# Kernel optimization log

Hardware: AMD Instinct MI355X
Metric: run time of the kernel (lower is better)

The kernel has to match this reference:

```python
import jax, jax.numpy as jnp
import numpy as np

B, S, D, H, E, K = 4, 2048, 768, 3072, 8, 2
LB_SCALE = 0.01
NOISY_STD = 1.0


def setup_inputs() -> dict:
    key = jax.random.key(0)
    ks = jax.random.split(key, 8)
    x = jax.random.normal(ks[0], (B, S, D), jnp.float32)
    # gate_linear: nn.Linear(D, E, bias=False); torch weight is [E, D]
    gate_w = jax.random.normal(ks[1], (E, D), jnp.float32) * 0.02
    noise_weight = jnp.zeros((E,), jnp.float32)  # initialized to zeros in torch
    noise = jax.random.normal(ks[2], (B, S, E), jnp.float32)  # torch.randn_like(logits)
    # expert weights stored in (in, out) layout: y = x @ w + b
    w1 = jax.random.normal(ks[3], (E, D, H), jnp.float32) * 0.02
    b1 = jnp.zeros((E, H), jnp.float32)
    w2 = jax.random.normal(ks[4], (E, D, H), jnp.float32) * 0.02
    b2 = jnp.zeros((E, H), jnp.float32)
    wp = jax.random.normal(ks[5], (E, H, D), jnp.float32) * 0.02
    bp = jnp.zeros((E, D), jnp.float32)
    return {"x": x, "gate_w": gate_w, "noise_weight": noise_weight, "noise": noise,
            "w1": w1, "b1": b1, "w2": w2, "b2": b2, "wp": wp, "bp": bp}


def reference(x, gate_w, noise_weight, noise, w1, b1, w2, b2, wp, bp):
    num_experts = gate_w.shape[0]
    # --- TopKGateParallel ---
    logits = jnp.einsum('bsd,ed->bse', x, gate_w)            # [B,S,E]
    gate_weights = jax.nn.softmax(logits, axis=-1)
    gate_weights_mean = gate_weights.reshape(-1, num_experts).mean(0)
    uniform = 1.0 / num_experts
    load_balance_loss = jnp.mean((gate_weights_mean - uniform) ** 2) * LB_SCALE
    logits_noisy = logits + noise * NOISY_STD * noise_weight  # noise_weight zeros => no-op at init
    top_k_vals, top_k_ids = jax.lax.top_k(logits_noisy, K)    # [B,S,K]
    # scatter top-k back into a -inf tensor, then softmax -> sparse gates
    topk_mask = jax.nn.one_hot(top_k_ids, num_experts, dtype=logits.dtype).sum(-2) > 0  # [B,S,E]
    sparse_logits = jnp.where(topk_mask, logits_noisy, -jnp.inf)
    gates = jax.nn.softmax(sparse_logits, axis=-1)            # zeros outside top-k
    # --- per-expert SwiGLU, weighted combine (gates are exactly 0 off top-k) ---
    y = jnp.zeros_like(x)
    for e in range(num_experts):  # small fixed expert count
        h = (x @ w1[e] + b1[e]) * jax.nn.silu(x @ w2[e] + b2[e])  # [B,S,H]
        y = y + gates[..., e:e + 1] * (h @ wp[e] + bp[e])
    return y, load_balance_loss
```

## Files before the change

### kernel.cpp

```cpp
#include <hip/hip_runtime.h>
#include <hip/hip_bf16.h>

#define NTOK 8192
#define DDIM 768
#define HDIM 3072
#define NEXP 8
#define MROWS (NTOK*2)

typedef float f32x4 __attribute__((ext_vector_type(4)));
typedef short bf16x8 __attribute__((ext_vector_type(8)));
typedef unsigned short u16x4 __attribute__((ext_vector_type(4)));

__device__ __forceinline__ unsigned short f2bf(float f) {
  union { float f; unsigned u; } v; v.f = f;
  unsigned r = v.u + 0x7fffu + ((v.u >> 16) & 1u);
  return (unsigned short)(r >> 16);
}

typedef __attribute__((address_space(3))) unsigned int* lds_ptr_t;
typedef const __attribute__((address_space(1))) unsigned int* gbl_ptr_t;
__device__ __forceinline__ void async16(const void* g, void* l) {
  __builtin_amdgcn_global_load_lds((gbl_ptr_t)g, (lds_ptr_t)l, 16, 0, 0);
}

__global__ __launch_bounds__(128) void gating_kernel(
    const float* __restrict__ x, const float* __restrict__ gw,
    const float* __restrict__ nw, const float* __restrict__ noise,
    int* counts, float* sums, int* tok_list, float* gate_list,
    int* tok_top, float* gate_top, int* pos_top)
{
  __shared__ float s_gw[NEXP*DDIM];
  __shared__ float s_sums[NEXP];
  __shared__ float s_nw[NEXP];
  int tid = threadIdx.x;
  for (int i = tid; i < NEXP*DDIM/4; i += 128)
    ((f32x4*)s_gw)[i] = ((const f32x4*)gw)[i];
  if (tid < NEXP) { s_sums[tid] = 0.f; s_nw[tid] = nw[tid]; }
  __syncthreads();
  int t = blockIdx.x*128 + tid;
  float acc[NEXP];
  #pragma unroll
  for (int e = 0; e < NEXP; ++e) acc[e] = 0.f;
  const f32x4* xr = (const f32x4*)(x + (size_t)t*DDIM);
  for (int d4 = 0; d4 < DDIM/4; ++d4) {
    f32x4 xv = xr[d4];
    #pragma unroll
    for (int e = 0; e < NEXP; ++e) {
      f32x4 g = *(const f32x4*)&s_gw[e*DDIM + d4*4];
      acc[e] += xv.x*g.x + xv.y*g.y + xv.z*g.z + xv.w*g.w;
    }
  }
  float m = acc[0];
  #pragma unroll
  for (int e = 1; e < NEXP; ++e) m = fmaxf(m, acc[e]);
  float p[NEXP], s = 0.f;
  #pragma unroll
  for (int e = 0; e < NEXP; ++e) { p[e] = __expf(acc[e]-m); s += p[e]; }
  float inv = 1.f/s;
  #pragma unroll
  for (int e = 0; e < NEXP; ++e) atomicAdd(&s_sums[e], p[e]*inv);
  float ln[NEXP];
  #pragma unroll
  for (int e = 0; e < NEXP; ++e) ln[e] = acc[e] + noise[(size_t)t*NEXP+e]*s_nw[e];
  int i0 = 0; float v0 = ln[0];
  #pragma unroll
  for (int e = 1; e < NEXP; ++e) if (ln[e] > v0) { v0 = ln[e]; i0 = e; }
  int i1 = -1; float v1 = 0.f;
  #pragma unroll
  for (int e = 0; e < NEXP; ++e)
    if (e != i0 && (i1 < 0 || ln[e] > v1)) { v1 = ln[e]; i1 = e; }
  float e1 = __expf(v1 - v0);
  float g0 = 1.f/(1.f + e1);
  float g1 = e1*g0;
  int p0 = atomicAdd(&counts[i0], 1);
  tok_list[i0*NTOK + p0] = t; gate_list[i0*NTOK + p0] = g0;
  int p1 = atomicAdd(&counts[i1], 1);
  tok_list[i1*NTOK + p1] = t; gate_list[i1*NTOK + p1] = g1;
  tok_top[2*t] = i0; tok_top[2*t+1] = i1;
  gate_top[2*t] = g0; gate_top[2*t+1] = g1;
  pos_top[2*t] = p0; pos_top[2*t+1] = p1;
  __syncthreads();
  if (tid < NEXP) atomicAdd(&sums[tid], s_sums[tid]);
}

__global__ void finalize_kernel(const int* counts, const float* sums,
                                int* offsets, float* loss_out)
{
  if (threadIdx.x == 0) {
    int o = 0;
    #pragma unroll
    for (int e = 0; e < NEXP; ++e) { offsets[e] = o; o += counts[e]; }
    offsets[NEXP] = o;
    float l = 0.f;
    #pragma unroll
    for (int e = 0; e < NEXP; ++e) {
      float dv = sums[e]*(1.f/(float)NTOK) - 1.f/(float)NEXP;
      l += dv*dv;
    }
    loss_out[0] = l*(0.01f/(float)NEXP);
  }
}

__global__ __launch_bounds__(256) void cvt_x_kernel(const float* __restrict__ x,
                                                    unsigned short* __restrict__ xb)
{
  int i = blockIdx.x*256 + threadIdx.x;
  f32x4 v = ((const f32x4*)x)[i];
  u16x4 o; o.x = f2bf(v.x); o.y = f2bf(v.y); o.z = f2bf(v.z); o.w = f2bf(v.w);
  ((u16x4*)xb)[i] = o;
}

__global__ __launch_bounds__(256) void transpose_cvt2_kernel(
    const float* __restrict__ src1, unsigned short* __restrict__ dst1,
    const float* __restrict__ src2, unsigned short* __restrict__ dst2,
    int R, int C)
{
  __shared__ unsigned short s[64*65];
  int z = blockIdx.z;
  int e = z & (NEXP-1);
  const float* src = (z < NEXP) ? src1 : src2;
  unsigned short* dst = (z < NEXP) ? dst1 : dst2;
  int r0 = blockIdx.y*64, c0 = blockIdx.x*64;
  const float* sp = src + ((size_t)e*R + r0)*C + c0;
  unsigned short* dp = dst + ((size_t)e*C + c0)*R + r0;
  int t = threadIdx.x;
  #pragma unroll
  for (int i = 0; i < 16; ++i) {
    int idx = t + 256*i;
    int r = idx >> 6, c = idx & 63;
    s[c*65 + r] = f2bf(sp[(size_t)r*C + c]);
  }
  __syncthreads();
  #pragma unroll
  for (int i = 0; i < 16; ++i) {
    int idx = t + 256*i;
    int c = idx >> 6, r = idx & 63;
    dp[(size_t)c*R + r] = s[c*65 + r];
  }
}

__global__ __launch_bounds__(256) void transpose_cvt_kernel(
    const float* __restrict__ src, unsigned short* __restrict__ dst, int R, int C)
{
  __shared__ unsigned short s[64*65];
  int e = blockIdx.z;
  int r0 = blockIdx.y*64, c0 = blockIdx.x*64;
  const float* sp = src + ((size_t)e*R + r0)*C + c0;
  unsigned short* dp = dst + ((size_t)e*C + c0)*R + r0;
  int t = threadIdx.x;
  #pragma unroll
  for (int i = 0; i < 16; ++i) {
    int idx = t + 256*i;
    int r = idx >> 6, c = idx & 63;
    s[c*65 + r] = f2bf(sp[(size_t)r*C + c]);
  }
  __syncthreads();
  #pragma unroll
  for (int i = 0; i < 16; ++i) {
    int idx = t + 256*i;
    int c = idx >> 6, r = idx & 63;
    dp[(size_t)c*R + r] = s[c*65 + r];
  }
}

__global__ __launch_bounds__(256) void compact_kernel(
    const int* __restrict__ counts, const int* __restrict__ offsets,
    const int* __restrict__ tok_list, const float* __restrict__ gate_list,
    int* __restrict__ row_token, float* __restrict__ row_gate)
{
  int e = blockIdx.y;
  int pos = blockIdx.x*256 + threadIdx.x;
  if (pos < counts[e]) {
    int r = offsets[e] + pos;
    row_token[r] = tok_list[e*NTOK + pos];
    row_gate[r]  = gate_list[e*NTOK + pos];
  }
}

__global__ __launch_bounds__(256) void init_y_kernel(
    const int* __restrict__ tok_top, const float* __restrict__ gate_top,
    const float* __restrict__ bp, float* __restrict__ y)
{
  int i = blockIdx.x*256 + threadIdx.x;
  int t = i / (DDIM/4);
  int d4 = i % (DDIM/4);
  int e0 = tok_top[2*t], e1 = tok_top[2*t+1];
  float g0 = gate_top[2*t], g1 = gate_top[2*t+1];
  f32x4 b0 = ((const f32x4*)(bp + (size_t)e0*DDIM))[d4];
  f32x4 b1v = ((const f32x4*)(bp + (size_t)e1*DDIM))[d4];
  ((f32x4*)y)[i] = g0*b0 + g1*b1v;
}

__global__ __launch_bounds__(256) void ffn1_mfma(
    const unsigned short* __restrict__ xb,
    const unsigned short* __restrict__ w1T, const unsigned short* __restrict__ w2T,
    const float* __restrict__ b1, const float* __restrict__ b2,
    const int* __restrict__ offsets, const int* __restrict__ row_token,
    unsigned short* __restrict__ h_buf, int h_base, int HC)
{
  int e = blockIdx.z;
  int r_lo = offsets[e];
  int rows_e = offsets[e+1] - r_lo;
  int bx = blockIdx.x;
  if (bx*128 >= rows_e) return;
  int r0 = r_lo + bx*128;
  int rows_valid = rows_e - bx*128; if (rows_valid > 128) rows_valid = 128;
  int h0 = h_base + blockIdx.y*64;

  __shared__ __align__(16) char sA[16384];
  __shared__ __align__(16) char sB[16384];
  __shared__ int s_tok[128];

  int tid = threadIdx.x;
  if (tid < 128) {
    int r = r0 + tid; if (r > MROWS-1) r = MROWS-1;
    s_tok[tid] = row_token[r];
  }
  __syncthreads();

  int lane = tid & 63, w = tid >> 6;
  int l16 = lane & 15, quad = lane >> 4;
  int lr = lane >> 2, ls = lane & 3;

  const unsigned short* gA[4]; char* lA[4];
  const unsigned short* gB[4]; char* lB[4];
  #pragma unroll
  for (int i = 0; i < 4; ++i) {
    int slot = i*4 + w;
    int chunk = slot & 7, kh = slot >> 3;
    gA[i] = xb + (size_t)s_tok[chunk*16 + lr]*DDIM + kh*32 + ls*8;
    lA[i] = sA + slot*1024;
    int mat = (slot >> 2) & 1;
    int col = h0 + w*16 + lr;
    const unsigned short* base = mat ? w2T : w1T;
    gB[i] = base + ((size_t)e*HDIM + col)*DDIM + kh*32 + ls*8;
    lB[i] = sB + slot*1024;
  }

  f32x4 acc1[8], acc2[8];
  #pragma unroll
  for (int i = 0; i < 8; ++i) { acc1[i] = (f32x4){0,0,0,0}; acc2[i] = (f32x4){0,0,0,0}; }

  int fro = l16*64 + quad*16;

  for (int k0 = 0; k0 < DDIM; k0 += 64) {
    #pragma unroll
    for (int i = 0; i < 4; ++i) async16(gA[i] + k0, lA[i]);
    #pragma unroll
    for (int i = 0; i < 4; ++i) async16(gB[i] + k0, lB[i]);
    __syncthreads();
    #pragma unroll
    for (int kh = 0; kh < 2; ++kh) {
      bf16x8 bf1 = *(const bf16x8*)(sB + (kh*8 + w)*1024 + fro);
      bf16x8 bf2 = *(const bf16x8*)(sB + (kh*8 + 4 + w)*1024 + fro);
      #pragma unroll
      for (int mt = 0; mt < 8; ++mt) {
        bf16x8 af = *(const bf16x8*)(sA + (kh*8 + mt)*1024 + fro);
        acc1[mt] = __builtin_amdgcn_mfma_f32_16x16x32_bf16(af, bf1, acc1[mt], 0, 0, 0);
        acc2[mt] = __builtin_amdgcn_mfma_f32_16x16x32_bf16(af, bf2, acc2[mt], 0, 0, 0);
      }
    }
    __syncthreads();
  }
  int hcol = h0 + w*16 + l16;
  float bb1 = b1[(size_t)e*HDIM + hcol];
  float bb2 = b2[(size_t)e*HDIM + hcol];
  int hl = hcol - h_base;
  #pragma unroll
  for (int mt = 0; mt < 8; ++mt) {
    #pragma unroll
    for (int r = 0; r < 4; ++r) {
      int row = mt*16 + quad*4 + r;
      if (row < rows_valid) {
        float c1 = acc1[mt][r] + bb1;
        float c2 = acc2[mt][r] + bb2;
        float hv = c1 * (c2 / (1.f + __expf(-c2)));
        h_buf[(size_t)(r0 + row)*HC + hl] = f2bf(hv);
      }
    }
  }
}

__global__ __launch_bounds__(256) void ffn2_mfma(
    const unsigned short* __restrict__ h_buf, const unsigned short* __restrict__ wpT,
    const int* __restrict__ offsets, const int* __restrict__ row_token,
    const float* __restrict__ row_gate, float* __restrict__ outp,
    int h_base, int HC, int mode)
{
  int e = blockIdx.z;
  int r_lo = offsets[e];
  int rows_e = offsets[e+1] - r_lo;
  int bx = blockIdx.x;
  if (bx*128 >= rows_e) return;
  int r0 = r_lo + bx*128;
  int rows_valid = rows_e - bx*128; if (rows_valid > 128) rows_valid = 128;
  int c0 = blockIdx.y*128;

  __shared__ __align__(16) char sA[16384];
  __shared__ __align__(16) char sB[16384];
  __shared__ int s_tok[128];
  __shared__ float s_gate[128];

  int tid = threadIdx.x;
  if (tid < 128) {
    int r = r0 + tid; if (r > MROWS-1) r = MROWS-1;
    s_tok[tid]  = row_token[r];
    s_gate[tid] = row_gate[r];
  }
  __syncthreads();

  int lane = tid & 63, w = tid >> 6;
  int l16 = lane & 15, quad = lane >> 4;
  int lr = lane >> 2, ls = lane & 3;
  int wr = w & 1, wcg = w >> 1;

  const unsigned short* gA[4]; char* lA[4];
  const unsigned short* gB[4]; char* lB[4];
  #pragma unroll
  for (int i = 0; i < 4; ++i) {
    int slot = i*4 + w;
    int chunk = slot & 7, kh = slot >> 3;
    int rr = r0 + chunk*16 + lr; if (rr > MROWS-1) rr = MROWS-1;
    gA[i] = h_buf + (size_t)rr*HC + kh*32 + ls*8;
    lA[i] = sA + slot*1024;
    int col = c0 + chunk*16 + lr;
    gB[i] = wpT + ((size_t)e*DDIM + col)*HDIM + h_base + kh*32 + ls*8;
    lB[i] = sB + slot*1024;
  }

  f32x4 acc[4][4];
  #pragma unroll
  for (int i = 0; i < 4; ++i)
    #pragma unroll
    for (int j = 0; j < 4; ++j) acc[i][j] = (f32x4){0,0,0,0};

  int fro = l16*64 + quad*16;

  for (int k0 = 0; k0 < HC; k0 += 64) {
    #pragma unroll
    for (int i = 0; i < 4; ++i) async16(gA[i] + k0, lA[i]);
    #pragma unroll
    for (int i = 0; i < 4; ++i) async16(gB[i] + k0, lB[i]);
    __syncthreads();
    #pragma unroll
    for (int kh = 0; kh < 2; ++kh) {
      bf16x8 bfr[4];
      #pragma unroll
      for (int nt = 0; nt < 4; ++nt)
        bfr[nt] = *(const bf16x8*)(sB + (kh*8 + wcg*4 + nt)*1024 + fro);
      #pragma unroll
      for (int mt = 0; mt < 4; ++mt) {
        bf16x8 af = *(const bf16x8*)(sA + (kh*8 + wr*4 + mt)*1024 + fro);
        #pragma unroll
        for (int nt = 0; nt < 4; ++nt)
          acc[mt][nt] = __builtin_amdgcn_mfma_f32_16x16x32_bf16(af, bfr[nt], acc[mt][nt], 0, 0, 0);
      }
    }
    __syncthreads();
  }

  if (mode == 0) {
    #pragma unroll
    for (int nt = 0; nt < 4; ++nt) {
      int col = c0 + wcg*64 + nt*16 + l16;
      #pragma unroll
      for (int mt = 0; mt < 4; ++mt) {
        #pragma unroll
        for (int r = 0; r < 4; ++r) {
          int row = wr*64 + mt*16 + quad*4 + r;
          if (row < rows_valid)
            outp[(size_t)(r0 + row)*DDIM + col] = acc[mt][nt][r];
        }
      }
    }
  } else {
    #pragma unroll
    for (int nt = 0; nt < 4; ++nt) {
      int col = c0 + wcg*64 + nt*16 + l16;
      #pragma unroll
      for (int mt = 0; mt < 4; ++mt) {
        #pragma unroll
        for (int r = 0; r < 4; ++r) {
          int row = wr*64 + mt*16 + quad*4 + r;
          if (row < rows_valid)
            atomicAdd(&outp[(size_t)s_tok[row]*DDIM + col], s_gate[row]*acc[mt][nt][r]);
        }
      }
    }
  }
}

__global__ __launch_bounds__(256) void combine_kernel(
    const float* __restrict__ part, const int* __restrict__ tok_top,
    const float* __restrict__ gate_top, const int* __restrict__ pos_top,
    const int* __restrict__ offsets, const float* __restrict__ bp,
    float* __restrict__ y)
{
  int i = blockIdx.x*256 + threadIdx.x;
  int t = i / (DDIM/4);
  int d4 = i % (DDIM/4);
  int e0 = tok_top[2*t], e1 = tok_top[2*t+1];
  float g0 = gate_top[2*t], g1 = gate_top[2*t+1];
  int r0 = offsets[e0] + pos_top[2*t];
  int r1 = offsets[e1] + pos_top[2*t+1];
  f32x4 v0 = ((const f32x4*)part)[(size_t)r0*(DDIM/4) + d4];
  f32x4 v1 = ((const f32x4*)part)[(size_t)r1*(DDIM/4) + d4];
  f32x4 b0 = ((const f32x4*)(bp + (size_t)e0*DDIM))[d4];
  f32x4 b1v = ((const f32x4*)(bp + (size_t)e1*DDIM))[d4];
  ((f32x4*)y)[i] = g0*(v0 + b0) + g1*(v1 + b1v);
}

__global__ __launch_bounds__(256) void ffn2_kernel(
    const unsigned short* __restrict__ h_buf, const float* __restrict__ wp,
    const int* __restrict__ offsets, const int* __restrict__ row_token,
    const float* __restrict__ row_gate, float* __restrict__ y, int h_base, int HC)
{
  int e = blockIdx.z;
  int r_lo = offsets[e];
  int rows_e = offsets[e+1] - r_lo;
  int bx = blockIdx.x;
  if (bx*128 >= rows_e) return;
  int r0 = r_lo + bx*128;
  int rows_valid = rows_e - bx*128; if (rows_valid > 128) rows_valid = 128;
  int c0 = blockIdx.y*128;

  __shared__ unsigned short sA[128*40];
  __shared__ int s_tok[128];
  __shared__ float s_gate[128];

  int tid = threadIdx.x;
  if (tid < 128) {
    int r = r0 + tid; if (r > MROWS-1) r = MROWS-1;
    s_tok[tid]  = row_token[r];
    s_gate[tid] = row_gate[r];
  }
  int lane = tid & 63;
  int wc = tid >> 6;
  int quad = lane >> 4, l16 = lane & 15;

  const float* wp0 = wp + (size_t)e*HDIM*DDIM + c0 + wc*32 + l16;

  f32x4 acc[8][2];
  #pragma unroll
  for (int i = 0; i < 8; ++i) { acc[i][0] = (f32x4){0,0,0,0}; acc[i][1] = (f32x4){0,0,0,0}; }
  __syncthreads();

  for (int k0 = 0; k0 < HC; k0 += 32) {
    #pragma unroll
    for (int i = 0; i < 2; ++i) {
      int c = i*256 + tid;
      int row = c >> 2, k8 = c & 3;
      int rr = r0 + row; if (rr > MROWS-1) rr = MROWS-1;
      bf16x8 v = *(const bf16x8*)(h_buf + (size_t)rr*HC + k0 + k8*8);
      *(bf16x8*)&sA[row*40 + k8*8] = v;
    }
    float bv[2][8];
    #pragma unroll
    for (int nt = 0; nt < 2; ++nt)
      #pragma unroll
      for (int j = 0; j < 8; ++j)
        bv[nt][j] = wp0[(size_t)(h_base + k0 + quad*8 + j)*DDIM + nt*16];
    bf16x8 bfr[2];
    #pragma unroll
    for (int nt = 0; nt < 2; ++nt)
      #pragma unroll
      for (int j = 0; j < 8; ++j) bfr[nt][j] = (short)f2bf(bv[nt][j]);
    __syncthreads();
    #pragma unroll
    for (int mt = 0; mt < 8; ++mt) {
      bf16x8 af = *(const bf16x8*)&sA[(mt*16 + l16)*40 + quad*8];
      acc[mt][0] = __builtin_amdgcn_mfma_f32_16x16x32_bf16(af, bfr[0], acc[mt][0], 0, 0, 0);
      acc[mt][1] = __builtin_amdgcn_mfma_f32_16x16x32_bf16(af, bfr[1], acc[mt][1], 0, 0, 0);
    }
    __syncthreads();
  }
  #pragma unroll
  for (int nt = 0; nt < 2; ++nt) {
    int col = c0 + wc*32 + nt*16 + l16;
    #pragma unroll
    for (int mt = 0; mt < 8; ++mt) {
      #pragma unroll
      for (int r = 0; r < 4; ++r) {
        int row = mt*16 + quad*4 + r;
        if (row < rows_valid)
          atomicAdd(&y[(size_t)s_tok[row]*DDIM + col], s_gate[row]*acc[mt][nt][r]);
      }
    }
  }
}

extern "C" void kernel_launch(void* const* d_in, const int* in_sizes, int n_in,
                              void* d_out, int out_size, void* d_ws, size_t ws_size,
                              hipStream_t stream)
{
  (void)in_sizes; (void)n_in; (void)out_size;
  const float* x     = (const float*)d_in[0];
  const float* gw    = (const float*)d_in[1];
  const float* nw    = (const float*)d_in[2];
  const float* noise = (const float*)d_in[3];
  const float* w1    = (const float*)d_in[4];
  const float* b1    = (const float*)d_in[5];
  const float* w2    = (const float*)d_in[6];
  const float* b2    = (const float*)d_in[7];
  const float* wp    = (const float*)d_in[8];
  const float* bp    = (const float*)d_in[9];
  float* y = (float*)d_out;

  char* ws = (char*)d_ws;
  int*   counts   = (int*)(ws + 0);
  float* sums     = (float*)(ws + 64);
  int*   offsets  = (int*)(ws + 128);
  size_t off = 256;
  int*   tok_list  = (int*)(ws + off);   off += (size_t)NEXP*NTOK*4;
  float* gate_list = (float*)(ws + off); off += (size_t)NEXP*NTOK*4;
  int*   tok_top   = (int*)(ws + off);   off += (size_t)NTOK*2*4;
  float* gate_top  = (float*)(ws + off); off += (size_t)NTOK*2*4;
  int*   pos_top   = (int*)(ws + off);   off += (size_t)NTOK*2*4;
  int*   row_token = (int*)(ws + off);   off += (size_t)MROWS*4;
  float* row_gate  = (float*)(ws + off); off += (size_t)MROWS*4;
  unsigned short* xb = (unsigned short*)(ws + off); off += (size_t)NTOK*DDIM*2;

  const size_t WT    = (size_t)NEXP*DDIM*HDIM*2;
  const size_t HFULL = (size_t)MROWS*HDIM*2;
  const size_t PSZ   = (size_t)MROWS*DDIM*4;

  unsigned short* w1T = (unsigned short*)(ws + off);
  unsigned short* w2T = (unsigned short*)(ws + off + WT);
  unsigned short* wpT = (unsigned short*)(ws + off + 2*WT);

  bool tierA = (off + 3*WT + HFULL + PSZ <= ws_size);
  bool haveP = (off + 3*WT + (size_t)MROWS*128*2 <= ws_size);
  size_t oH = off + (haveP ? 3*WT : 2*WT);

  int HC;
  unsigned short* h_buf;
  float* part = nullptr;
  if (tierA) {
    HC = HDIM;
    h_buf = (unsigned short*)(ws + off + 3*WT);
    part  = (float*)(ws + off + 3*WT + HFULL);
  } else {
    static const int hc_opts[6] = {3072, 1536, 768, 384, 192, 128};
    HC = 128;
    for (int i = 0; i < 6; ++i)
      if (oH + (size_t)MROWS*hc_opts[i]*2 <= ws_size) { HC = hc_opts[i]; break; }
    h_buf = (unsigned short*)(ws + oH);
  }

  hipMemsetAsync(d_ws, 0, 256, stream);
  cvt_x_kernel<<<NTOK*DDIM/1024, 256, 0, stream>>>(x, xb);
  transpose_cvt2_kernel<<<dim3(HDIM/64, DDIM/64, NEXP*2), 256, 0, stream>>>(
      w1, w1T, w2, w2T, DDIM, HDIM);
  if (haveP)
    transpose_cvt_kernel<<<dim3(DDIM/64, HDIM/64, NEXP), 256, 0, stream>>>(wp, wpT, HDIM, DDIM);

  gating_kernel<<<NTOK/128, 128, 0, stream>>>(x, gw, nw, noise, counts, sums,
                                              tok_list, gate_list, tok_top, gate_top, pos_top);
  finalize_kernel<<<1, 64, 0, stream>>>(counts, sums, offsets, y + (size_t)NTOK*DDIM);
  compact_kernel<<<dim3(NTOK/256, NEXP), 256, 0, stream>>>(counts, offsets, tok_list,
                                                           gate_list, row_token, row_gate);

  if (tierA) {
    ffn1_mfma<<<dim3(128, HDIM/64, NEXP), 256, 0, stream>>>(xb, w1T, w2T, b1, b2, offsets,
                                                            row_token, h_buf, 0, HC);
    ffn2_mfma<<<dim3(128, DDIM/128, NEXP), 256, 0, stream>>>(h_buf, wpT, offsets, row_token,
                                                             row_gate, part, 0, HC, 0);
    combine_kernel<<<NTOK*DDIM/1024, 256, 0, stream>>>(part, tok_top, gate_top, pos_top,
                                                       offsets, bp, y);
  } else {
    init_y_kernel<<<NTOK*DDIM/1024, 256, 0, stream>>>(tok_top, gate_top, bp, y);
    int nch = HDIM / HC;
    for (int c = 0; c < nch; ++c) {
      ffn1_mfma<<<dim3(128, HC/64, NEXP), 256, 0, stream>>>(xb, w1T, w2T, b1, b2, offsets,
                                                            row_token, h_buf, c*HC, HC);
      if (haveP)
        ffn2_mfma<<<dim3(128, DDIM/128, NEXP), 256, 0, stream>>>(h_buf, wpT, offsets, row_token,
                                                                 row_gate, y, c*HC, HC, 1);
      else
        ffn2_kernel<<<dim3(128, DDIM/128, NEXP), 256, 0, stream>>>(h_buf, wp, offsets, row_token,
                                                                   row_gate, y, c*HC, HC);
    }
  }
}
```

Measured before the change: 1.006 ms.

## Use persistent row-block loops, XOR-swizzled LDS, and K=32 steps in expert GEMMs

The grouped FFN GEMM kernels now launch a compact 1D grid: the expert index is interleaved into the block id, and each block loops over row blocks with a stride of 32. This replaces the old 128-row-block grid, in which most blocks returned immediately. The K step drops from 64 to 32, halving LDS tiles to 8KB so more blocks can fit per CU. An XOR swizzle on the global load segment and the fragment read offset is meant to avoid LDS bank conflicts. The trade-off is twice as many barrier pairs per K, and a block serialises its row blocks whenever an expert receives more than 32 of them.

```diff
diff --git a/kernel.cpp b/kernel.cpp
--- a/kernel.cpp
+++ b/kernel.cpp
@@ -6,6 +6,7 @@
 #define HDIM 3072
 #define NEXP 8
 #define MROWS (NTOK*2)
+#define RBMAX 32
 
 typedef float f32x4 __attribute__((ext_vector_type(4)));
 typedef short bf16x8 __attribute__((ext_vector_type(8)));
@@ -198,84 +199,82 @@
     const int* __restrict__ offsets, const int* __restrict__ row_token,
     unsigned short* __restrict__ h_buf, int h_base, int HC)
 {
-  int e = blockIdx.z;
+  int id = blockIdx.x;
+  int e = id & 7;
+  int s = id >> 3;
+  int rb0 = s & (RBMAX-1);
+  int cg = s >> 5;
   int r_lo = offsets[e];
   int rows_e = offsets[e+1] - r_lo;
-  int bx = blockIdx.x;
-  if (bx*128 >= rows_e) return;
-  int r0 = r_lo + bx*128;
-  int rows_valid = rows_e - bx*128; if (rows_valid > 128) rows_valid = 128;
-  int h0 = h_base + blockIdx.y*64;
-
-  __shared__ __align__(16) char sA[16384];
-  __shared__ __align__(16) char sB[16384];
+  int h0 = h_base + cg*64;
+
+  __shared__ __align__(16) char sA[8192];
+  __shared__ __align__(16) char sB[8192];
   __shared__ int s_tok[128];
 
   int tid = threadIdx.x;
-  if (tid < 128) {
-    int r = r0 + tid; if (r > MROWS-1) r = MROWS-1;
-    s_tok[tid] = row_token[r];
-  }
-  __syncthreads();
-
   int lane = tid & 63, w = tid >> 6;
   int l16 = lane & 15, quad = lane >> 4;
   int lr = lane >> 2, ls = lane & 3;
-
-  const unsigned short* gA[4]; char* lA[4];
-  const unsigned short* gB[4]; char* lB[4];
-  #pragma unroll
-  for (int i = 0; i < 4; ++i) {
-    int slot = i*4 + w;
-    int chunk = slot & 7, kh = slot >> 3;
-    gA[i] = xb + (size_t)s_tok[chunk*16 + lr]*DDIM + kh*32 + ls*8;
-    lA[i] = sA + slot*1024;
-    int mat = (slot >> 2) & 1;
-    int col = h0 + w*16 + lr;
-    const unsigned short* base = mat ? w2T : w1T;
-    gB[i] = base + ((size_t)e*HDIM + col)*DDIM + kh*32 + ls*8;
-    lB[i] = sB + slot*1024;
-  }
-
-  f32x4 acc1[8], acc2[8];
-  #pragma unroll
-  for (int i = 0; i < 8; ++i) { acc1[i] = (f32x4){0,0,0,0}; acc2[i] = (f32x4){0,0,0,0}; }
-
-  int fro = l16*64 + quad*16;
-
-  for (int k0 = 0; k0 < DDIM; k0 += 64) {
-    #pragma unroll
-    for (int i = 0; i < 4; ++i) async16(gA[i] + k0, lA[i]);
-    #pragma unroll
-    for (int i = 0; i < 4; ++i) async16(gB[i] + k0, lB[i]);
-    __syncthreads();
-    #pragma unroll
-    for (int kh = 0; kh < 2; ++kh) {
-      bf16x8 bf1 = *(const bf16x8*)(sB + (kh*8 + w)*1024 + fro);
-      bf16x8 bf2 = *(const bf16x8*)(sB + (kh*8 + 4 + w)*1024 + fro);
-      #pragma unroll
-      for (int mt = 0; mt < 8; ++mt) {
-        bf16x8 af = *(const bf16x8*)(sA + (kh*8 + mt)*1024 + fro);
-        acc1[mt] = __builtin_amdgcn_mfma_f32_16x16x32_bf16(af, bf1, acc1[mt], 0, 0, 0);
-        acc2[mt] = __builtin_amdgcn_mfma_f32_16x16x32_bf16(af, bf2, acc2[mt], 0, 0, 0);
-      }
-    }
-    __syncthreads();
-  }
+  int kseg = ls ^ (lr & 3);
+  int fro = l16*64 + ((quad ^ (l16 & 3)) << 4);
+
+  int colB = h0 + w*16 + lr;
+  const unsigned short* gB1 = w1T + ((size_t)e*HDIM + colB)*DDIM + kseg*8;
+  const unsigned short* gB2 = w2T + ((size_t)e*HDIM + colB)*DDIM + kseg*8;
+  char* lA0 = sA + w*1024;
+  char* lA1 = sA + (w+4)*1024;
+  char* lB1 = sB + w*1024;
+  char* lB2 = sB + (w+4)*1024;
+
   int hcol = h0 + w*16 + l16;
   float bb1 = b1[(size_t)e*HDIM + hcol];
   float bb2 = b2[(size_t)e*HDIM + hcol];
   int hl = hcol - h_base;
-  #pragma unroll
-  for (int mt = 0; mt < 8; ++mt) {
-    #pragma unroll
-    for (int r = 0; r < 4; ++r) {
-      int row = mt*16 + quad*4 + r;
-      if (row < rows_valid) {
-        float c1 = acc1[mt][r] + bb1;
-        float c2 = acc2[mt][r] + bb2;
-        float hv = c1 * (c2 / (1.f + __expf(-c2)));
-        h_buf[(size_t)(r0 + row)*HC + hl] = f2bf(hv);
+
+  for (int rb = rb0; rb*128 < rows_e; rb += RBMAX) {
+    int r0 = r_lo + rb*128;
+    int rows_valid = rows_e - rb*128; if (rows_valid > 128) rows_valid = 128;
+    __syncthreads();
+    if (tid < 128) {
+      int r = r0 + tid; if (r > MROWS-1) r = MROWS-1;
+      s_tok[tid] = row_token[r];
+    }
+    __syncthreads();
+    const unsigned short* gA0 = xb + (size_t)s_tok[w*16 + lr]*DDIM + kseg*8;
+    const unsigned short* gA1 = xb + (size_t)s_tok[(w+4)*16 + lr]*DDIM + kseg*8;
+
+    f32x4 acc1[8], acc2[8];
+    #pragma unroll
+    for (int i = 0; i < 8; ++i) { acc1[i] = (f32x4){0,0,0,0}; acc2[i] = (f32x4){0,0,0,0}; }
+
+    for (int k0 = 0; k0 < DDIM; k0 += 32) {
+      async16(gA0 + k0, lA0);
+      async16(gA1 + k0, lA1);
+      async16(gB1 + k0, lB1);
+      async16(gB2 + k0, lB2);
+      __syncthreads();
+      bf16x8 bf1 = *(const bf16x8*)(sB + w*1024 + fro);
+      bf16x8 bf2 = *(const bf16x8*)(sB + (w+4)*1024 + fro);
+      #pragma unroll
+      for (int mt = 0; mt < 8; ++mt) {
+        bf16x8 af = *(const bf16x8*)(sA + mt*1024 + fro);
+        acc1[mt] = __builtin_amdgcn_mfma_f32_16x16x32_bf16(af, bf1, acc1[mt], 0, 0, 0);
+        acc2[mt] = __builtin_amdgcn_mfma_f32_16x16x32_bf16(af, bf2, acc2[mt], 0, 0, 0);
+      }
+      __syncthreads();
+    }
+    #pragma unroll
+    for (int mt = 0; mt < 8; ++mt) {
+      #pragma unroll
+      for (int r = 0; r < 4; ++r) {
+        int row = mt*16 + quad*4 + r;
+        if (row < rows_valid) {
+          float c1 = acc1[mt][r] + bb1;
+          float c2 = acc2[mt][r] + bb2;
+          float hv = c1 * (c2 / (1.f + __expf(-c2)));
+          h_buf[(size_t)(r0 + row)*HC + hl] = f2bf(hv);
+        }
       }
     }
   }
@@ -287,103 +286,102 @@
     const float* __restrict__ row_gate, float* __restrict__ outp,
     int h_base, int HC, int mode)
 {
-  int e = blockIdx.z;
+  int id = blockIdx.x;
+  int e = id & 7;
+  int s = id >> 3;
+  int rb0 = s & (RBMAX-1);
+  int cb = s >> 5;
   int r_lo = offsets[e];
   int rows_e = offsets[e+1] - r_lo;
-  int bx = blockIdx.x;
-  if (bx*128 >= rows_e) return;
-  int r0 = r_lo + bx*128;
-  int rows_valid = rows_e - bx*128; if (rows_valid > 128) rows_valid = 128;
-  int c0 = blockIdx.y*128;
-
-  __shared__ __align__(16) char sA[16384];
-  __shared__ __align__(16) char sB[16384];
+  int c0 = cb*128;
+
+  __shared__ __align__(16) char sA[8192];
+  __shared__ __align__(16) char sB[8192];
   __shared__ int s_tok[128];
   __shared__ float s_gate[128];
 
   int tid = threadIdx.x;
-  if (tid < 128) {
-    int r = r0 + tid; if (r > MROWS-1) r = MROWS-1;
-    s_tok[tid]  = row_token[r];
-    s_gate[tid] = row_gate[r];
-  }
-  __syncthreads();
-
   int lane = tid & 63, w = tid >> 6;
   int l16 = lane & 15, quad = lane >> 4;
   int lr = lane >> 2, ls = lane & 3;
+  int kseg = ls ^ (lr & 3);
+  int fro = l16*64 + ((quad ^ (l16 & 3)) << 4);
   int wr = w & 1, wcg = w >> 1;
 
-  const unsigned short* gA[4]; char* lA[4];
-  const unsigned short* gB[4]; char* lB[4];
-  #pragma unroll
-  for (int i = 0; i < 4; ++i) {
-    int slot = i*4 + w;
-    int chunk = slot & 7, kh = slot >> 3;
-    int rr = r0 + chunk*16 + lr; if (rr > MROWS-1) rr = MROWS-1;
-    gA[i] = h_buf + (size_t)rr*HC + kh*32 + ls*8;
-    lA[i] = sA + slot*1024;
-    int col = c0 + chunk*16 + lr;
-    gB[i] = wpT + ((size_t)e*DDIM + col)*HDIM + h_base + kh*32 + ls*8;
-    lB[i] = sB + slot*1024;
-  }
-
-  f32x4 acc[4][4];
-  #pragma unroll
-  for (int i = 0; i < 4; ++i)
-    #pragma unroll
-    for (int j = 0; j < 4; ++j) acc[i][j] = (f32x4){0,0,0,0};
-
-  int fro = l16*64 + quad*16;
-
-  for (int k0 = 0; k0 < HC; k0 += 64) {
-    #pragma unroll
-    for (int i = 0; i < 4; ++i) async16(gA[i] + k0, lA[i]);
-    #pragma unroll
-    for (int i = 0; i < 4; ++i) async16(gB[i] + k0, lB[i]);
+  const unsigned short* gB0 = wpT + ((size_t)e*DDIM + c0 + w*16 + lr)*HDIM + h_base + kseg*8;
+  const unsigned short* gB1 = wpT + ((size_t)e*DDIM + c0 + (w+4)*16 + lr)*HDIM + h_base + kseg*8;
+  char* lA0 = sA + w*1024;
+  char* lA1 = sA + (w+4)*1024;
+  char* lB0 = sB + w*1024;
+  char* lB1 = sB + (w+4)*1024;
+
+  for (int rb = rb0; rb*128 < rows_e; rb += RBMAX) {
+    int r0 = r_lo + rb*128;
+    int rows_valid = rows_e - rb*128; if (rows_valid > 128) rows_valid = 128;
     __syncthreads();
-    #pragma unroll
-    for (int kh = 0; kh < 2; ++kh) {
+    if (tid < 128) {
+      int r = r0 + tid; if (r > MROWS-1) r = MROWS-1;
+      s_tok[tid]  = row_token[r];
+      s_gate[tid] = row_gate[r];
+    }
+    __syncthreads();
+    int rA0 = r0 + w*16 + lr;     if (rA0 > MROWS-1) rA0 = MROWS-1;
+    int rA1 = r0 + (w+4)*16 + lr; if (rA1 > MROWS-1) rA1 = MROWS-1;
+    const unsigned short* gA0 = h_buf + (size_t)rA0*HC + kseg*8;
+    const unsigned short* gA1 = h_buf + (size_t)rA1*HC + kseg*8;
+
+    f32x4 acc[4][4];
+    #pragma unroll
+    for (int i = 0; i < 4; ++i)
+      #pragma unroll
+      for (int j = 0; j < 4; ++j) acc[i][j] = (f32x4){0,0,0,0};
+
+    for (int k0 = 0; k0 < HC; k0 += 32) {
+      async16(gA0 + k0, lA0);
+      async16(gA1 + k0, lA1);
+      async16(gB0 + k0, lB0);
+      async16(gB1 + k0, lB1);
+      __syncthreads();
       bf16x8 bfr[4];
       #pragma unroll
       for (int nt = 0; nt < 4; ++nt)
-        bfr[nt] = *(const bf16x8*)(sB + (kh*8 + wcg*4 + nt)*1024 + fro);
+        bfr[nt] = *(const bf16x8*)(sB + (wcg*4 + nt)*1024 + fro);
       #pragma unroll
       for (int mt = 0; mt < 4; ++mt) {
-        bf16x8 af = *(const bf16x8*)(sA + (kh*8 + wr*4 + mt)*1024 + fro);
+        bf16x8 af = *(const bf16x8*)(sA + (wr*4 + mt)*1024 + fro);
         #pragma unroll
         for (int nt = 0; nt < 4; ++nt)
           acc[mt][nt] = __builtin_amdgcn_mfma_f32_16x16x32_bf16(af, bfr[nt], acc[mt][nt], 0, 0, 0);
       }
-    }
-    __syncthreads();
-  }
-
-  if (mode == 0) {
-    #pragma unroll
-    for (int nt = 0; nt < 4; ++nt) {
-      int col = c0 + wcg*64 + nt*16 + l16;
-      #pragma unroll
-      for (int mt = 0; mt < 4; ++mt) {
+      __syncthreads();
+    }
+
+    if (mode == 0) {
+      #pragma unroll
+      for (int nt = 0; nt < 4; ++nt) {
+        int col = c0 + wcg*64 + nt*16 + l16;
         #pragma unroll
-        for (int r = 0; r < 4; ++r) {
-          int row = wr*64 + mt*16 + quad*4 + r;
-          if (row < rows_valid)
-            outp[(size_t)(r0 + row)*DDIM + col] = acc[mt][nt][r];
+        for (int mt = 0; mt < 4; ++mt) {
+          #pragma unroll
+          for (int r = 0; r < 4; ++r) {
+            int row = wr*64 + mt*16 + quad*4 + r;
+            if (row < rows_valid)
+              outp[(size_t)(r0 + row)*DDIM + col] = acc[mt][nt][r];
+          }
         }
       }
-    }
-  } else {
-    #pragma unroll
-    for (int nt = 0; nt < 4; ++nt) {
-      int col = c0 + wcg*64 + nt*16 + l16;
-      #pragma unroll
-      for (int mt = 0; mt < 4; ++mt) {
+    } else {
+      #pragma unroll
+      for (int nt = 0; nt < 4; ++nt) {
+        int col = c0 + wcg*64 + nt*16 + l16;
         #pragma unroll
-        for (int r = 0; r < 4; ++r) {
-          int row = wr*64 + mt*16 + quad*4 + r;
-          if (row < rows_valid)
-            atomicAdd(&outp[(size_t)s_tok[row]*DDIM + col], s_gate[row]*acc[mt][nt][r]);
+        for (int mt = 0; mt < 4; ++mt) {
+          #pragma unroll
+          for (int r = 0; r < 4; ++r) {
+            int row = wr*64 + mt*16 + quad*4 + r;
+            if (row < rows_valid)
+              atomicAdd(&outp[(size_t)s_tok[row]*DDIM + col], s_gate[row]*acc[mt][nt][r]);
+          }
         }
       }
     }
@@ -561,21 +559,21 @@
                                                            gate_list, row_token, row_gate);
 
   if (tierA) {
-    ffn1_mfma<<<dim3(128, HDIM/64, NEXP), 256, 0, stream>>>(xb, w1T, w2T, b1, b2, offsets,
-                                                            row_token, h_buf, 0, HC);
-    ffn2_mfma<<<dim3(128, DDIM/128, NEXP), 256, 0, stream>>>(h_buf, wpT, offsets, row_token,
-                                                             row_gate, part, 0, HC, 0);
+    ffn1_mfma<<<NEXP*(HDIM/64)*RBMAX, 256, 0, stream>>>(xb, w1T, w2T, b1, b2, offsets,
+                                                        row_token, h_buf, 0, HC);
+    ffn2_mfma<<<NEXP*(DDIM/128)*RBMAX, 256, 0, stream>>>(h_buf, wpT, offsets, row_token,
+                                                         row_gate, part, 0, HC, 0);
     combine_kernel<<<NTOK*DDIM/1024, 256, 0, stream>>>(part, tok_top, gate_top, pos_top,
                                                        offsets, bp, y);
   } else {
     init_y_kernel<<<NTOK*DDIM/1024, 256, 0, stream>>>(tok_top, gate_top, bp, y);
     int nch = HDIM / HC;
     for (int c = 0; c < nch; ++c) {
-      ffn1_mfma<<<dim3(128, HC/64, NEXP), 256, 0, stream>>>(xb, w1T, w2T, b1, b2, offsets,
-                                                            row_token, h_buf, c*HC, HC);
+      ffn1_mfma<<<NEXP*(HC/64)*RBMAX, 256, 0, stream>>>(xb, w1T, w2T, b1, b2, offsets,
+                                                        row_token, h_buf, c*HC, HC);
       if (haveP)
-        ffn2_mfma<<<dim3(128, DDIM/128, NEXP), 256, 0, stream>>>(h_buf, wpT, offsets, row_token,
-                                                                 row_gate, y, c*HC, HC, 1);
+        ffn2_mfma<<<NEXP*(DDIM/128)*RBMAX, 256, 0, stream>>>(h_buf, wpT, offsets, row_token,
+                                                             row_gate, y, c*HC, HC, 1);
       else
         ffn2_kernel<<<dim3(128, DDIM/128, NEXP), 256, 0, stream>>>(h_buf, wp, offsets, row_token,
                                                                    row_gate, y, c*HC, HC);
```

Measured after the change: 823.8 us. -18.1%, faster.
